# Optimization experiments

Hardware: AMD Instinct MI355X
Metric: run time of the kernel (lower is better)

Reference implementation:

```python
import jax, jax.numpy as jnp
import numpy as np

B, C, H, W = 4, 256, 64, 64
CQK = C // 8


def setup_inputs() -> dict:
    key = jax.random.key(0)
    ks = jax.random.split(key, 7)
    s = 1.0 / np.sqrt(C)
    return {
        "x": jax.random.normal(ks[0], (B, C, H, W), dtype=jnp.float32),
        "Wq": jax.random.normal(ks[1], (CQK, C), dtype=jnp.float32) * s,
        "bq": jax.random.normal(ks[2], (CQK,), dtype=jnp.float32) * 0.01,
        "Wk": jax.random.normal(ks[3], (CQK, C), dtype=jnp.float32) * s,
        "bk": jax.random.normal(ks[4], (CQK,), dtype=jnp.float32) * 0.01,
        "Wv": jax.random.normal(ks[5], (C, C), dtype=jnp.float32) * s,
        "bv": jax.random.normal(ks[6], (C,), dtype=jnp.float32) * 0.01,
    }


def reference(x, Wq, bq, Wk, bk, Wv, bv):
    b, c, h, w = x.shape
    n = h * w
    xf = x.reshape(b, c, n)                                   # [B,C,N]
    # 1x1 convs == per-pixel channel projections
    q = jnp.einsum('oc,bcn->bon', Wq, xf) + bq[None, :, None]  # [B,C/8,N]
    k = jnp.einsum('oc,bcn->bon', Wk, xf) + bk[None, :, None]  # [B,C/8,N]
    v = jnp.einsum('oc,bcn->bon', Wv, xf) + bv[None, :, None]  # [B,C,N]
    # energy[b,i,j] = <q[:, i], k[:, j]>  (no scaling, as in the original)
    energy = jnp.einsum('boi,boj->bij', q, k)                  # [B,N,N]
    attn = jax.nn.softmax(energy, axis=-1)                     # [B,N,N]
    # out[b,c,i] = sum_j v[b,c,j] * attn[b,i,j]
    out = jnp.einsum('bcj,bij->bci', v, attn)                  # [B,C,N]
    return out.reshape(b, c, h, w) + x
```

## Files before the change

### kernel.cpp

```cpp
#include <hip/hip_runtime.h>
#include <hip/hip_bf16.h>
#include <math.h>

#define B_DIM 4
#define C_DIM 256
#define CQK_DIM 32
#define N_POS 4096
#define NPART 4

typedef unsigned short u16;
typedef __attribute__((ext_vector_type(8))) short bf16x8;
typedef __attribute__((ext_vector_type(4))) float f32x4;

__device__ __forceinline__ u16 f32_to_bf16_rn(float f) {
    union { float f; unsigned int u; } v; v.f = f;
    unsigned int u = v.u;
    u += 0x7fffu + ((u >> 16) & 1u);
    return (u16)(u >> 16);
}
__device__ __forceinline__ float bf16_to_f32(u16 h) {
    union { unsigned int u; float f; } v; v.u = ((unsigned int)h) << 16;
    return v.f;
}
__device__ __forceinline__ unsigned pk_bf16(float a, float b) {
    unsigned r;
    asm("v_cvt_pk_bf16_f32 %0, %1, %2" : "=v"(r) : "v"(a), "v"(b));
    return r;
}
__device__ __forceinline__ void async_copy16(const u16* g, u16* l) {
    __builtin_amdgcn_global_load_lds(
        (const __attribute__((address_space(1))) void*)g,
        (__attribute__((address_space(3))) void*)l, 16, 0, 0);
}


__global__ __launch_bounds__(256) void proj_kernel(
    const float* __restrict__ x,
    const float* __restrict__ Wq, const float* __restrict__ bq,
    const float* __restrict__ Wk, const float* __restrict__ bk,
    const float* __restrict__ Wv, const float* __restrict__ bv,
    u16* __restrict__ qhi, u16* __restrict__ qlo,
    u16* __restrict__ kth, u16* __restrict__ ktl,
    u16* __restrict__ vtile)
{
    const int t    = threadIdx.x;
    const int blk  = blockIdx.x;
    const int b    = blk >> 6;
    const int jt   = blk & 63;
    const int n0   = jt * 64;
    const int wave = t >> 6;
    const int lane = t & 63;
    const int n16  = lane & 15;
    const int quad = lane >> 4;
    const float* xb = x + (size_t)b * C_DIM * N_POS;

    f32x4 accV[4][4];
    f32x4 accQ[4];
    #pragma unroll
    for (int v = 0; v < 4; ++v)
        #pragma unroll
        for (int nt = 0; nt < 4; ++nt) accV[v][nt] = (f32x4){0.f,0.f,0.f,0.f};
    #pragma unroll
    for (int nt = 0; nt < 4; ++nt) accQ[nt] = (f32x4){0.f,0.f,0.f,0.f};

    const float* Wqk  = (wave < 2) ? Wq : Wk;
    const int    qkrow = (wave & 1) * 16 + n16;

    for (int kk = 0; kk < 8; ++kk) {
        const int k0 = kk * 32 + quad * 8;
        bf16x8 bh[4], bl[4];
        #pragma unroll
        for (int nt = 0; nt < 4; ++nt) {
            const float* xp = xb + (size_t)k0 * N_POS + n0 + nt * 16 + n16;
            float xv[8];
            #pragma unroll
            for (int j = 0; j < 8; ++j) xv[j] = xp[(size_t)j * N_POS];
            #pragma unroll
            for (int j = 0; j < 8; ++j) {
                u16 h = f32_to_bf16_rn(xv[j]);
                bh[nt][j] = (short)h;
                bl[nt][j] = (short)f32_to_bf16_rn(xv[j] - bf16_to_f32(h));
            }
        }
        #pragma unroll
        for (int v = 0; v < 4; ++v) {
            const float* wr = Wv + (size_t)(wave * 64 + v * 16 + n16) * C_DIM + k0;
            float4 a0 = *(const float4*)(wr);
            float4 a1 = *(const float4*)(wr + 4);
            bf16x8 ah;
            ah[0] = (short)f32_to_bf16_rn(a0.x); ah[1] = (short)f32_to_bf16_rn(a0.y);
            ah[2] = (short)f32_to_bf16_rn(a0.z); ah[3] = (short)f32_to_bf16_rn(a0.w);
            ah[4] = (short)f32_to_bf16_rn(a1.x); ah[5] = (short)f32_to_bf16_rn(a1.y);
            ah[6] = (short)f32_to_bf16_rn(a1.z); ah[7] = (short)f32_to_bf16_rn(a1.w);
            #pragma unroll
            for (int nt = 0; nt < 4; ++nt)
                accV[v][nt] = __builtin_amdgcn_mfma_f32_16x16x32_bf16(
                    ah, bh[nt], accV[v][nt], 0, 0, 0);
        }
        {
            const float* wr = Wqk + (size_t)qkrow * C_DIM + k0;
            bf16x8 ah, al;
            #pragma unroll
            for (int j = 0; j < 8; ++j) {
                float w = wr[j];
                u16 h = f32_to_bf16_rn(w);
                ah[j] = (short)h;
                al[j] = (short)f32_to_bf16_rn(w - bf16_to_f32(h));
            }
            #pragma unroll
            for (int nt = 0; nt < 4; ++nt) {
                accQ[nt] = __builtin_amdgcn_mfma_f32_16x16x32_bf16(ah, bh[nt], accQ[nt], 0, 0, 0);
                accQ[nt] = __builtin_amdgcn_mfma_f32_16x16x32_bf16(ah, bl[nt], accQ[nt], 0, 0, 0);
                accQ[nt] = __builtin_amdgcn_mfma_f32_16x16x32_bf16(al, bh[nt], accQ[nt], 0, 0, 0);
            }
        }
    }

    u16* vt = vtile + (size_t)(b * 64 + jt) * (32 * 512);
    #pragma unroll
    for (int v = 0; v < 4; ++v) {
        const int cb = wave * 4 + v;
        #pragma unroll
        for (int r = 0; r < 4; ++r) {
            const int c = cb * 16 + quad * 4 + r;
            const float bias = bv[c];
            #pragma unroll
            for (int nt = 0; nt < 4; ++nt) {
                const int kb = nt >> 1;
                vt[(cb * 2 + kb) * 512
                   + ((n16 >> 2) * 16 + quad * 4 + r) * 8
                   + (nt & 1) * 4 + (n16 & 3)] =
                    f32_to_bf16_rn(accV[v][nt][r] + bias);
            }
        }
    }
    if (wave < 2) {
        #pragma unroll
        for (int r = 0; r < 4; ++r) {
            const int c = (wave & 1) * 16 + quad * 4 + r;
            const float bias = bq[c];
            #pragma unroll
            for (int nt = 0; nt < 4; ++nt) {
                float val = accQ[nt][r] + bias;
                u16 h = f32_to_bf16_rn(val);
                u16 lo = f32_to_bf16_rn(val - bf16_to_f32(h));
                size_t base = ((size_t)b * N_POS + n0 + nt * 16 + n16) * CQK_DIM + c;
                qhi[base] = h; qlo[base] = lo;
            }
        }
    } else {
        u16* kh_t = kth + (size_t)(b * 64 + jt) * (4 * 512);
        u16* kl_t = ktl + (size_t)(b * 64 + jt) * (4 * 512);
        #pragma unroll
        for (int r = 0; r < 4; ++r) {
            const int c = (wave & 1) * 16 + quad * 4 + r;
            const float bias = bk[c];
            #pragma unroll
            for (int nt = 0; nt < 4; ++nt) {
                float val = accQ[nt][r] + bias;
                u16 h = f32_to_bf16_rn(val);
                u16 lo = f32_to_bf16_rn(val - bf16_to_f32(h));
                const int off = nt * 512 + ((c >> 3) * 16 + n16) * 8 + (c & 7);
                kh_t[off] = h; kl_t[off] = lo;
            }
        }
    }
}

__global__ __launch_bounds__(256, 2) void flash_kernel(
    const u16* __restrict__ qhi, const u16* __restrict__ qlo,
    const u16* __restrict__ kth, const u16* __restrict__ ktl,
    const u16* __restrict__ vtile,
    u16* __restrict__ part, float2* __restrict__ ml)
{
    __shared__ u16 Vt[2][40 * 512];

    const int t    = threadIdx.x;
    const int wave = t >> 6;
    const int lane = t & 63;
    const int n16  = lane & 15;
    const int quad = lane >> 4;

    const int idx    = blockIdx.x;
    const int xcd    = idx & 7;
    const int b      = xcd & 3;
    const int z      = idx >> 3;
    const int p      = z & 3;
    const int iouter = z >> 2;
    const int itile  = (iouter << 1) | (xcd >> 2);
    const int i0     = itile * 128 + wave * 32;

    bf16x8 qh[2], ql[2];
    #pragma unroll
    for (int m = 0; m < 2; ++m) {
        qh[m] = *(const bf16x8*)(qhi + ((size_t)b * N_POS + i0 + m * 16 + n16) * CQK_DIM + quad * 8);
        ql[m] = *(const bf16x8*)(qlo + ((size_t)b * N_POS + i0 + m * 16 + n16) * CQK_DIM + quad * 8);
    }

    f32x4 O[2][16];
    #pragma unroll
    for (int m = 0; m < 2; ++m)
        #pragma unroll
        for (int cb = 0; cb < 16; ++cb) O[m][cb] = (f32x4){0.f, 0.f, 0.f, 0.f};
    float lsum[2] = {0.f, 0.f};

    const int jt_beg = p * 16;
    const int jt_end = jt_beg + 16;

    const u16* vb_base = vtile + (size_t)b * 64 * (32 * 512);
    const u16* kh_base = kth   + (size_t)b * 64 * (4 * 512);
    const u16* kl_base = ktl   + (size_t)b * 64 * (4 * 512);

#define STAGE(JT, BUF)                                                          \
    {                                                                           \
        const u16* vsrc  = vb_base + (size_t)(JT) * (32 * 512);                 \
        const u16* khsrc = kh_base + (size_t)(JT) * (4 * 512);                  \
        const u16* klsrc = kl_base + (size_t)(JT) * (4 * 512);                  \
        for (int ch = wave; ch < 32; ch += 4)                                   \
            async_copy16(vsrc + ch * 512 + lane * 8, Vt[BUF] + ch * 512);       \
        for (int ch = wave; ch < 8; ch += 4)                                    \
            async_copy16((ch < 4 ? khsrc + ch * 512 : klsrc + (ch - 4) * 512)   \
                             + lane * 8,                                        \
                         Vt[BUF] + (32 + ch) * 512);                            \
    }

    STAGE(jt_beg, 0);

    int buf = 0;
    for (int jt = jt_beg; jt < jt_end; ++jt) {
        __syncthreads();

        if (jt + 1 < jt_end) STAGE(jt + 1, buf ^ 1);

        const u16* kbuf = Vt[buf];
        bf16x8 kh[4], kl[4];
        #pragma unroll
        for (int jb = 0; jb < 4; ++jb) {
            kh[jb] = *(const bf16x8*)(kbuf + (32 + jb) * 512 + lane * 8);
            kl[jb] = *(const bf16x8*)(kbuf + (36 + jb) * 512 + lane * 8);
        }

        f32x4 s[2][4];
        __builtin_amdgcn_s_setprio(1);
        #pragma unroll
        for (int m = 0; m < 2; ++m)
            #pragma unroll
            for (int jb = 0; jb < 4; ++jb) {
                f32x4 acc = (f32x4){0.f, 0.f, 0.f, 0.f};
                acc = __builtin_amdgcn_mfma_f32_16x16x32_bf16(kh[jb], qh[m], acc, 0, 0, 0);
                acc = __builtin_amdgcn_mfma_f32_16x16x32_bf16(kl[jb], qh[m], acc, 0, 0, 0);
                acc = __builtin_amdgcn_mfma_f32_16x16x32_bf16(kh[jb], ql[m], acc, 0, 0, 0);
                s[m][jb] = acc;
            }
        __builtin_amdgcn_s_setprio(0);

        bf16x8 Pf[2][2];
        #pragma unroll
        for (int m = 0; m < 2; ++m)
            #pragma unroll
            for (int kb = 0; kb < 2; ++kb) {
                union { bf16x8 v; unsigned u[4]; } tmp;
                #pragma unroll
                for (int j2 = 0; j2 < 2; ++j2) {
                    const int jb = kb * 2 + j2;
                    float p0 = __expf(s[m][jb][0]);
                    float p1 = __expf(s[m][jb][1]);
                    float p2 = __expf(s[m][jb][2]);
                    float p3 = __expf(s[m][jb][3]);
                    lsum[m] += (p0 + p1) + (p2 + p3);
                    tmp.u[j2 * 2 + 0] = pk_bf16(p0, p1);
                    tmp.u[j2 * 2 + 1] = pk_bf16(p2, p3);
                }
                Pf[m][kb] = tmp.v;
            }

        const u16* vb = Vt[buf];
        __builtin_amdgcn_s_setprio(1);
        #pragma unroll
        for (int kb = 0; kb < 2; ++kb) {
            #pragma unroll
            for (int cb = 0; cb < 16; ++cb) {
                bf16x8 Vf = *(const bf16x8*)(vb + (cb * 2 + kb) * 512 + lane * 8);
                #pragma unroll
                for (int m = 0; m < 2; ++m)
                    O[m][cb] = __builtin_amdgcn_mfma_f32_16x16x32_bf16(
                        Pf[m][kb], Vf, O[m][cb], 0, 0, 0);
            }
        }
        __builtin_amdgcn_s_setprio(0);
        buf ^= 1;
    }
#undef STAGE

    #pragma unroll
    for (int m = 0; m < 2; ++m) {
        lsum[m] += __shfl_xor(lsum[m], 16, 64);
        lsum[m] += __shfl_xor(lsum[m], 32, 64);
    }
    float inv_l[2][4];
    #pragma unroll
    for (int m = 0; m < 2; ++m)
        #pragma unroll
        for (int r = 0; r < 4; ++r)
            inv_l[m][r] = 1.f / __shfl(lsum[m], quad * 4 + r, 64);

    u16* pbase = part + ((size_t)(p * 4 + b) * N_POS + i0) * C_DIM;
    #pragma unroll
    for (int m = 0; m < 2; ++m)
        #pragma unroll
        for (int cb = 0; cb < 16; ++cb)
            #pragma unroll
            for (int r = 0; r < 4; ++r)
                pbase[(size_t)(m * 16 + quad * 4 + r) * C_DIM + cb * 16 + n16] =
                    f32_to_bf16_rn(O[m][cb][r] * inv_l[m][r]);
    if (quad == 0) {
        #pragma unroll
        for (int m = 0; m < 2; ++m)
            ml[(size_t)(p * 4 + b) * N_POS + i0 + m * 16 + n16] =
                make_float2(0.f, lsum[m]);
    }
}

__global__ __launch_bounds__(256) void reduce_kernel(
    const u16* __restrict__ part, const float2* __restrict__ ml,
    const float* __restrict__ x, float* __restrict__ out)
{
    const int TJ = 32;
    __shared__ float wgt[NPART][TJ];
    __shared__ float trans[C_DIM][TJ + 1];

    const int t   = threadIdx.x;
    const int blk = blockIdx.x;
    const int b   = blk >> 7;
    const int n0  = (blk & 127) * TJ;

    if (t < TJ) {
        int i = n0 + t;
        float s = 0.f, w[NPART];
        #pragma unroll
        for (int p = 0; p < NPART; ++p) {
            float2 a = ml[(size_t)(p * 4 + b) * N_POS + i];
            w[p] = a.y;
            s += w[p];
        }
        float inv = 1.f / s;
        #pragma unroll
        for (int p = 0; p < NPART; ++p) wgt[p][t] = w[p] * inv;
    }
    __syncthreads();

    {
        const int cp = t & 127;
        const int ih = t >> 7;
        for (int ib = 0; ib < TJ; ib += 2) {
            int i = ib + ih;
            float acc0 = 0.f, acc1 = 0.f;
            #pragma unroll
            for (int p = 0; p < NPART; ++p) {
                const u16* row = part + ((size_t)(p * 4 + b) * N_POS + n0 + i) * C_DIM;
                ushort2 pv = ((const ushort2*)row)[cp];
                float wp = wgt[p][i];
                acc0 += wp * bf16_to_f32(pv.x);
                acc1 += wp * bf16_to_f32(pv.y);
            }
            trans[2 * cp][i]     = acc0;
            trans[2 * cp + 1][i] = acc1;
        }
    }
    __syncthreads();

    {
        const int il = t & 31;
        const int cr = t >> 5;
        const float* xb = x + (size_t)b * C_DIM * N_POS;
        float* ob       = out + (size_t)b * C_DIM * N_POS;
        for (int cc = 0; cc < 32; ++cc) {
            int c = cc * 8 + cr;
            size_t g = (size_t)c * N_POS + n0 + il;
            ob[g] = trans[c][il] + xb[g];
        }
    }
}

extern "C" void kernel_launch(void* const* d_in, const int* in_sizes, int n_in,
                              void* d_out, int out_size, void* d_ws, size_t ws_size,
                              hipStream_t stream) {
    const float* x  = (const float*)d_in[0];
    const float* Wq = (const float*)d_in[1];
    const float* bq = (const float*)d_in[2];
    const float* Wk = (const float*)d_in[3];
    const float* bk = (const float*)d_in[4];
    const float* Wv = (const float*)d_in[5];
    const float* bv = (const float*)d_in[6];
    float* out = (float*)d_out;

    char* ws = (char*)d_ws;
    u16*    qhi   = (u16*)(ws);
    u16*    qlo   = (u16*)(ws + (1ull << 20));
    u16*    kth   = (u16*)(ws + (2ull << 20));
    u16*    ktl   = (u16*)(ws + (3ull << 20));
    u16*    vtile = (u16*)(ws + (4ull << 20));
    u16*    part  = (u16*)(ws + (12ull << 20));
    float2* mlp   = (float2*)(ws + (44ull << 20));

    hipLaunchKernelGGL(proj_kernel, dim3(256), dim3(256), 0, stream,
                       x, Wq, bq, Wk, bk, Wv, bv, qhi, qlo, kth, ktl, vtile);
    hipLaunchKernelGGL(flash_kernel, dim3(512), dim3(256), 0, stream,
                       qhi, qlo, kth, ktl, vtile, part, mlp);
    hipLaunchKernelGGL(reduce_kernel, dim3(512), dim3(256), 0, stream,
                       part, mlp, x, out);
}
```

Baseline: 88.51 us.

## Halve flash query tile and key step to raise occupancy

```diff
diff --git a/kernel.cpp b/kernel.cpp
--- a/kernel.cpp
+++ b/kernel.cpp
@@ -167,13 +167,13 @@
     }
 }
 
-__global__ __launch_bounds__(256, 2) void flash_kernel(
+__global__ __launch_bounds__(256, 4) void flash_kernel(
     const u16* __restrict__ qhi, const u16* __restrict__ qlo,
     const u16* __restrict__ kth, const u16* __restrict__ ktl,
     const u16* __restrict__ vtile,
     u16* __restrict__ part, float2* __restrict__ ml)
 {
-    __shared__ u16 Vt[2][40 * 512];
+    __shared__ u16 Vt[2][20 * 512];
 
     const int t    = threadIdx.x;
     const int wave = t >> 6;
@@ -188,137 +188,111 @@
     const int p      = z & 3;
     const int iouter = z >> 2;
     const int itile  = (iouter << 1) | (xcd >> 2);
-    const int i0     = itile * 128 + wave * 32;
-
-    bf16x8 qh[2], ql[2];
-    #pragma unroll
-    for (int m = 0; m < 2; ++m) {
-        qh[m] = *(const bf16x8*)(qhi + ((size_t)b * N_POS + i0 + m * 16 + n16) * CQK_DIM + quad * 8);
-        ql[m] = *(const bf16x8*)(qlo + ((size_t)b * N_POS + i0 + m * 16 + n16) * CQK_DIM + quad * 8);
-    }
-
-    f32x4 O[2][16];
-    #pragma unroll
-    for (int m = 0; m < 2; ++m)
-        #pragma unroll
-        for (int cb = 0; cb < 16; ++cb) O[m][cb] = (f32x4){0.f, 0.f, 0.f, 0.f};
-    float lsum[2] = {0.f, 0.f};
-
-    const int jt_beg = p * 16;
-    const int jt_end = jt_beg + 16;
+    const int i0     = itile * 64 + wave * 16;
+
+    bf16x8 qh, ql;
+    qh = *(const bf16x8*)(qhi + ((size_t)b * N_POS + i0 + n16) * CQK_DIM + quad * 8);
+    ql = *(const bf16x8*)(qlo + ((size_t)b * N_POS + i0 + n16) * CQK_DIM + quad * 8);
+
+    f32x4 O[16];
+    #pragma unroll
+    for (int cb = 0; cb < 16; ++cb) O[cb] = (f32x4){0.f, 0.f, 0.f, 0.f};
+    float lsum = 0.f;
+
+    const int j_beg = p * 32;
+    const int j_end = j_beg + 32;
 
     const u16* vb_base = vtile + (size_t)b * 64 * (32 * 512);
     const u16* kh_base = kth   + (size_t)b * 64 * (4 * 512);
     const u16* kl_base = ktl   + (size_t)b * 64 * (4 * 512);
 
-#define STAGE(JT, BUF)                                                          \
+#define STAGE(J32, BUF)                                                         \
     {                                                                           \
-        const u16* vsrc  = vb_base + (size_t)(JT) * (32 * 512);                 \
-        const u16* khsrc = kh_base + (size_t)(JT) * (4 * 512);                  \
-        const u16* klsrc = kl_base + (size_t)(JT) * (4 * 512);                  \
-        for (int ch = wave; ch < 32; ch += 4)                                   \
-            async_copy16(vsrc + ch * 512 + lane * 8, Vt[BUF] + ch * 512);       \
-        for (int ch = wave; ch < 8; ch += 4)                                    \
-            async_copy16((ch < 4 ? khsrc + ch * 512 : klsrc + (ch - 4) * 512)   \
-                             + lane * 8,                                        \
-                         Vt[BUF] + (32 + ch) * 512);                            \
-    }
-
-    STAGE(jt_beg, 0);
+        const int jt64 = (J32) >> 1;                                            \
+        const int kb   = (J32) & 1;                                             \
+        const u16* vsrc  = vb_base + (size_t)jt64 * (32 * 512);                 \
+        const u16* khsrc = kh_base + (size_t)jt64 * (4 * 512) + kb * 2 * 512;   \
+        const u16* klsrc = kl_base + (size_t)jt64 * (4 * 512) + kb * 2 * 512;   \
+        for (int ch = wave; ch < 20; ch += 4) {                                 \
+            const u16* g = (ch < 16) ? vsrc + (ch * 2 + kb) * 512               \
+                         : (ch < 18) ? khsrc + (ch - 16) * 512                  \
+                                     : klsrc + (ch - 18) * 512;                 \
+            async_copy16(g + lane * 8, Vt[BUF] + ch * 512);                     \
+        }                                                                       \
+    }
+
+    STAGE(j_beg, 0);
 
     int buf = 0;
-    for (int jt = jt_beg; jt < jt_end; ++jt) {
+    for (int j32 = j_beg; j32 < j_end; ++j32) {
         __syncthreads();
 
-        if (jt + 1 < jt_end) STAGE(jt + 1, buf ^ 1);
+        if (j32 + 1 < j_end) STAGE(j32 + 1, buf ^ 1);
 
         const u16* kbuf = Vt[buf];
-        bf16x8 kh[4], kl[4];
-        #pragma unroll
-        for (int jb = 0; jb < 4; ++jb) {
-            kh[jb] = *(const bf16x8*)(kbuf + (32 + jb) * 512 + lane * 8);
-            kl[jb] = *(const bf16x8*)(kbuf + (36 + jb) * 512 + lane * 8);
-        }
-
-        f32x4 s[2][4];
+        bf16x8 kh[2], kl[2];
+        #pragma unroll
+        for (int jb = 0; jb < 2; ++jb) {
+            kh[jb] = *(const bf16x8*)(kbuf + (16 + jb) * 512 + lane * 8);
+            kl[jb] = *(const bf16x8*)(kbuf + (18 + jb) * 512 + lane * 8);
+        }
+
+        f32x4 s[2];
         __builtin_amdgcn_s_setprio(1);
         #pragma unroll
-        for (int m = 0; m < 2; ++m)
-            #pragma unroll
-            for (int jb = 0; jb < 4; ++jb) {
-                f32x4 acc = (f32x4){0.f, 0.f, 0.f, 0.f};
-                acc = __builtin_amdgcn_mfma_f32_16x16x32_bf16(kh[jb], qh[m], acc, 0, 0, 0);
-                acc = __builtin_amdgcn_mfma_f32_16x16x32_bf16(kl[jb], qh[m], acc, 0, 0, 0);
-                acc = __builtin_amdgcn_mfma_f32_16x16x32_bf16(kh[jb], ql[m], acc, 0, 0, 0);
-                s[m][jb] = acc;
-            }
+        for (int jb = 0; jb < 2; ++jb) {
+            f32x4 acc = (f32x4){0.f, 0.f, 0.f, 0.f};
+            acc = __builtin_amdgcn_mfma_f32_16x16x32_bf16(kh[jb], qh, acc, 0, 0, 0);
+            acc = __builtin_amdgcn_mfma_f32_16x16x32_bf16(kl[jb], qh, acc, 0, 0, 0);
+            acc = __builtin_amdgcn_mfma_f32_16x16x32_bf16(kh[jb], ql, acc, 0, 0, 0);
+            s[jb] = acc;
+        }
         __builtin_amdgcn_s_setprio(0);
 
-        bf16x8 Pf[2][2];
-        #pragma unroll
-        for (int m = 0; m < 2; ++m)
-            #pragma unroll
-            for (int kb = 0; kb < 2; ++kb) {
-                union { bf16x8 v; unsigned u[4]; } tmp;
-                #pragma unroll
-                for (int j2 = 0; j2 < 2; ++j2) {
-                    const int jb = kb * 2 + j2;
-                    float p0 = __expf(s[m][jb][0]);
-                    float p1 = __expf(s[m][jb][1]);
-                    float p2 = __expf(s[m][jb][2]);
-                    float p3 = __expf(s[m][jb][3]);
-                    lsum[m] += (p0 + p1) + (p2 + p3);
-                    tmp.u[j2 * 2 + 0] = pk_bf16(p0, p1);
-                    tmp.u[j2 * 2 + 1] = pk_bf16(p2, p3);
-                }
-                Pf[m][kb] = tmp.v;
-            }
+        bf16x8 Pf;
+        {
+            union { bf16x8 v; unsigned u[4]; } tmp;
+            #pragma unroll
+            for (int jb = 0; jb < 2; ++jb) {
+                float p0 = __expf(s[jb][0]);
+                float p1 = __expf(s[jb][1]);
+                float p2 = __expf(s[jb][2]);
+                float p3 = __expf(s[jb][3]);
+                lsum += (p0 + p1) + (p2 + p3);
+                tmp.u[jb * 2 + 0] = pk_bf16(p0, p1);
+                tmp.u[jb * 2 + 1] = pk_bf16(p2, p3);
+            }
+            Pf = tmp.v;
+        }
 
         const u16* vb = Vt[buf];
         __builtin_amdgcn_s_setprio(1);
         #pragma unroll
-        for (int kb = 0; kb < 2; ++kb) {
-            #pragma unroll
-            for (int cb = 0; cb < 16; ++cb) {
-                bf16x8 Vf = *(const bf16x8*)(vb + (cb * 2 + kb) * 512 + lane * 8);
-                #pragma unroll
-                for (int m = 0; m < 2; ++m)
-                    O[m][cb] = __builtin_amdgcn_mfma_f32_16x16x32_bf16(
-                        Pf[m][kb], Vf, O[m][cb], 0, 0, 0);
-            }
+        for (int cb = 0; cb < 16; ++cb) {
+            bf16x8 Vf = *(const bf16x8*)(vb + cb * 512 + lane * 8);
+            O[cb] = __builtin_amdgcn_mfma_f32_16x16x32_bf16(Pf, Vf, O[cb], 0, 0, 0);
         }
         __builtin_amdgcn_s_setprio(0);
         buf ^= 1;
     }
 #undef STAGE
 
-    #pragma unroll
-    for (int m = 0; m < 2; ++m) {
-        lsum[m] += __shfl_xor(lsum[m], 16, 64);
-        lsum[m] += __shfl_xor(lsum[m], 32, 64);
-    }
-    float inv_l[2][4];
-    #pragma unroll
-    for (int m = 0; m < 2; ++m)
+    lsum += __shfl_xor(lsum, 16, 64);
+    lsum += __shfl_xor(lsum, 32, 64);
+    float inv_l[4];
+    #pragma unroll
+    for (int r = 0; r < 4; ++r)
+        inv_l[r] = 1.f / __shfl(lsum, quad * 4 + r, 64);
+
+    u16* pbase = part + ((size_t)(p * 4 + b) * N_POS + i0) * C_DIM;
+    #pragma unroll
+    for (int cb = 0; cb < 16; ++cb)
         #pragma unroll
         for (int r = 0; r < 4; ++r)
-            inv_l[m][r] = 1.f / __shfl(lsum[m], quad * 4 + r, 64);
-
-    u16* pbase = part + ((size_t)(p * 4 + b) * N_POS + i0) * C_DIM;
-    #pragma unroll
-    for (int m = 0; m < 2; ++m)
-        #pragma unroll
-        for (int cb = 0; cb < 16; ++cb)
-            #pragma unroll
-            for (int r = 0; r < 4; ++r)
-                pbase[(size_t)(m * 16 + quad * 4 + r) * C_DIM + cb * 16 + n16] =
-                    f32_to_bf16_rn(O[m][cb][r] * inv_l[m][r]);
-    if (quad == 0) {
-        #pragma unroll
-        for (int m = 0; m < 2; ++m)
-            ml[(size_t)(p * 4 + b) * N_POS + i0 + m * 16 + n16] =
-                make_float2(0.f, lsum[m]);
-    }
+            pbase[(size_t)(quad * 4 + r) * C_DIM + cb * 16 + n16] =
+                f32_to_bf16_rn(O[cb][r] * inv_l[r]);
+    if (quad == 0)
+        ml[(size_t)(p * 4 + b) * N_POS + i0 + n16] = make_float2(0.f, lsum);
 }
 
 __global__ __launch_bounds__(256) void reduce_kernel(
@@ -405,7 +379,7 @@
 
     hipLaunchKernelGGL(proj_kernel, dim3(256), dim3(256), 0, stream,
                        x, Wq, bq, Wk, bk, Wv, bv, qhi, qlo, kth, ktl, vtile);
-    hipLaunchKernelGGL(flash_kernel, dim3(512), dim3(256), 0, stream,
+    hipLaunchKernelGGL(flash_kernel, dim3(1024), dim3(256), 0, stream,
                        qhi, qlo, kth, ktl, vtile, part, mlp);
     hipLaunchKernelGGL(reduce_kernel, dim3(512), dim3(256), 0, stream,
                        part, mlp, x, out);
```

After: 97.56 us. 1.1x slower.
